# Kernel tuning notes

Measured on AMD Instinct MI355X. Metric: run time of the kernel, lower is better.

The kernel has to match this reference:

```python
import jax, jax.numpy as jnp
import numpy as np

EPS = 1e-5
NUM_GROUPS = 8


def group_norm(x, gamma, beta):
    # x: [B, C, T]; normalize per group over (C/G, T)
    B, C, T = x.shape
    G = NUM_GROUPS
    xg = x.reshape(B, G, C // G, T)
    mean = xg.mean(axis=(2, 3), keepdims=True)
    var = xg.var(axis=(2, 3), keepdims=True)
    xn = ((xg - mean) * jax.lax.rsqrt(var + EPS)).reshape(B, C, T)
    return xn * gamma[None, :, None] + beta[None, :, None]


def mish(x):
    return x * jnp.tanh(jax.nn.softplus(x))


def setup_inputs() -> dict:
    key = jax.random.key(0)
    ks = jax.random.split(key, 7)
    C, Cb, B, T = 1024, 256, 64, 512
    # conv1d kernel_size=1 weights stored as [out, in]
    w_down = jax.random.normal(ks[0], (Cb, C), dtype=jnp.float32) / np.sqrt(C)
    b_down = jax.random.normal(ks[1], (Cb,), dtype=jnp.float32) * 0.01
    w_up = jax.random.normal(ks[2], (C, Cb), dtype=jnp.float32) / np.sqrt(Cb)
    b_up = jax.random.normal(ks[3], (C,), dtype=jnp.float32) * 0.01
    gamma = jnp.ones((C,), dtype=jnp.float32)
    beta = jnp.zeros((C,), dtype=jnp.float32)
    x = jax.random.normal(ks[4], (B, C, T), dtype=jnp.float32)
    return {"x": x, "gamma": gamma, "beta": beta,
            "w_down": w_down, "b_down": b_down,
            "w_up": w_up, "b_up": b_up}


def reference(x, gamma, beta, w_down, b_down, w_up, b_up):
    residual = x
    h = group_norm(x, gamma, beta)                       # [B, C, T]
    h = jnp.einsum('bct,oc->bot', h, w_down) + b_down[None, :, None]  # [B, Cb, T]
    h = mish(h)
    h = jnp.einsum('bct,oc->bot', h, w_up) + b_up[None, :, None]      # [B, C, T]
    return h + residual
```

## Files before the change

### kernel.cpp

```cpp
#include <hip/hip_runtime.h>
#include <hip/hip_bf16.h>
#include <stddef.h>

#define B_   64
#define C_   1024
#define CB_  256
#define T_   512
#define G_   8
#define N_   32768
#define EPS_ 1e-5f

using short8  = __attribute__((ext_vector_type(8))) short;
using short4v = __attribute__((ext_vector_type(4))) short;
using f32x4   = __attribute__((ext_vector_type(4))) float;

__device__ __forceinline__ short f2bf(float f) {
    unsigned u = __float_as_uint(f);
    u += 0x7fffu + ((u >> 16) & 1u);
    return (short)(u >> 16);
}

__device__ __forceinline__ float mish_f(float y) {
    float u = __expf(fminf(y, 30.f));
    float w = u * u + 2.f * u;
    return y * (w / (w + 2.f));
}

__global__ void prep_weights(const float* __restrict__ wd, const float* __restrict__ wu,
                             short* __restrict__ wdb, short* __restrict__ wut) {
    int i = blockIdx.x * 256 + threadIdx.x;
    if (i < CB_ * C_) {
        wdb[i] = f2bf(wd[i]);
        int m = i >> 8, k = i & 255;
        int idx = (((m >> 4) * 8 + (k >> 5)) << 9) + (((k >> 3) & 3) << 7)
                + ((m & 15) << 3) + (k & 7);
        wut[idx] = f2bf(wu[i]);
    }
}

__global__ void stats_kernel(const float* __restrict__ x, const float* __restrict__ gamma,
                             const float* __restrict__ beta,
                             float* __restrict__ scaleW, float* __restrict__ shiftW) {
    const int tid = threadIdx.x;
    const int bg = blockIdx.x;
    const int b = bg >> 3, g = bg & 7;
    const float4* p = (const float4*)(x + ((size_t)b * C_ + g * 128) * T_);
    float s = 0.f, q = 0.f;
    for (int i = tid; i < 16384; i += 256) {
        float4 v = p[i];
        s += v.x + v.y + v.z + v.w;
        q += v.x * v.x + v.y * v.y + v.z * v.z + v.w * v.w;
    }
    for (int o = 32; o > 0; o >>= 1) {
        s += __shfl_down(s, o);
        q += __shfl_down(q, o);
    }
    __shared__ float red[8];
    __shared__ float mr[2];
    const int wid = tid >> 6, lane = tid & 63;
    if (lane == 0) { red[wid] = s; red[4 + wid] = q; }
    __syncthreads();
    if (tid == 0) {
        float S = red[0] + red[1] + red[2] + red[3];
        float Q = red[4] + red[5] + red[6] + red[7];
        float mean = S * (1.f / 65536.f);
        float var = Q * (1.f / 65536.f) - mean * mean;
        mr[0] = mean;
        mr[1] = rsqrtf(var + EPS_);
    }
    __syncthreads();
    float mean = mr[0], rstd = mr[1];
    if (tid < 128) {
        int c = g * 128 + tid;
        float sc = rstd * gamma[c];
        scaleW[b * C_ + c] = sc;
        shiftW[b * C_ + c] = beta[c] - mean * sc;
    }
}

#define LDSTR 40
#define MSTR  264

__global__ __launch_bounds__(512, 2) void fused_adapter(
    const float* __restrict__ x, const short* __restrict__ wd,
    const float* __restrict__ b_down,
    const float* __restrict__ scaleW, const float* __restrict__ shiftW,
    const short* __restrict__ wut, const float* __restrict__ b_up,
    float* __restrict__ out) {
    __shared__ short As[256 * LDSTR];
    __shared__ short Bs[128 * LDSTR];
    __shared__ float sS[C_], sT[C_];
    __shared__ short Ms[128 * MSTR];

    const int tid = threadIdx.x;
    const int n0 = blockIdx.x * 128;
    const int b  = n0 >> 9;
    const int t0 = n0 & 511;

    for (int i = tid; i < C_; i += 512) {
        sS[i] = scaleW[b * C_ + i];
        sT[i] = shiftW[b * C_ + i];
    }

    const int a_kc = tid & 3;
    const int a_m  = tid >> 2;
    const int b_n  = tid & 127;
    const int b_kg = tid >> 7;
    const int wid  = tid >> 6;
    const int lane = tid & 63;
    const int wm = wid >> 1, wn = wid & 1;
    const int q = lane >> 4, l16 = lane & 15;

    f32x4 acc[4][4];
#pragma unroll
    for (int i = 0; i < 4; i++)
#pragma unroll
        for (int j = 0; j < 4; j++) acc[i][j] = 0.f;

    const float* xb = x + (size_t)b * C_ * T_ + t0;

    short8 a0, a1;
    float bv[8];
    {
        const short* src = wd + a_m * C_ + a_kc * 8;
        a0 = *(const short8*)src;
        a1 = *(const short8*)(src + 128 * C_);
        const float* xp = xb + (size_t)(b_kg * 8) * T_ + b_n;
#pragma unroll
        for (int i = 0; i < 8; i++) bv[i] = xp[(size_t)i * T_];
    }
    __syncthreads();
    {
        *(short8*)&As[a_m * LDSTR + a_kc * 8] = a0;
        *(short8*)&As[(a_m + 128) * LDSTR + a_kc * 8] = a1;
        short8 v;
        const int kb = b_kg * 8;
#pragma unroll
        for (int i = 0; i < 8; i++) v[i] = f2bf(bv[i] * sS[kb + i] + sT[kb + i]);
        *(short8*)&Bs[b_n * LDSTR + kb] = v;
    }
    __syncthreads();

    for (int kt = 0; kt < 32; ++kt) {
        if (kt < 31) {
            const int k1 = (kt + 1) * 32;
            const short* src = wd + a_m * C_ + k1 + a_kc * 8;
            a0 = *(const short8*)src;
            a1 = *(const short8*)(src + 128 * C_);
            const float* xp = xb + (size_t)(k1 + b_kg * 8) * T_ + b_n;
#pragma unroll
            for (int i = 0; i < 8; i++) bv[i] = xp[(size_t)i * T_];
        }
        short8 af[4], bfr[4];
#pragma unroll
        for (int i = 0; i < 4; i++)
            af[i] = *(const short8*)&As[(wm * 64 + i * 16 + l16) * LDSTR + q * 8];
#pragma unroll
        for (int j = 0; j < 4; j++)
            bfr[j] = *(const short8*)&Bs[(wn * 64 + j * 16 + l16) * LDSTR + q * 8];
#pragma unroll
        for (int i = 0; i < 4; i++)
#pragma unroll
            for (int j = 0; j < 4; j++)
                acc[i][j] = __builtin_amdgcn_mfma_f32_16x16x32_bf16(af[i], bfr[j], acc[i][j], 0, 0, 0);
        __syncthreads();
        if (kt < 31) {
            *(short8*)&As[a_m * LDSTR + a_kc * 8] = a0;
            *(short8*)&As[(a_m + 128) * LDSTR + a_kc * 8] = a1;
            short8 v;
            const int kb = (kt + 1) * 32 + b_kg * 8;
            const int kl = b_kg * 8;
#pragma unroll
            for (int i = 0; i < 8; i++) v[i] = f2bf(bv[i] * sS[kb + i] + sT[kb + i]);
            *(short8*)&Bs[b_n * LDSTR + kl] = v;
        }
        __syncthreads();
    }

#pragma unroll
    for (int i = 0; i < 4; i++) {
        const int o_b = wm * 64 + i * 16 + q * 4;
        const float bd0 = b_down[o_b];
        const float bd1 = b_down[o_b + 1];
        const float bd2 = b_down[o_b + 2];
        const float bd3 = b_down[o_b + 3];
#pragma unroll
        for (int j = 0; j < 4; j++) {
            const int nl = wn * 64 + j * 16 + l16;
            short4v v;
            v[0] = f2bf(mish_f(acc[i][j][0] + bd0));
            v[1] = f2bf(mish_f(acc[i][j][1] + bd1));
            v[2] = f2bf(mish_f(acc[i][j][2] + bd2));
            v[3] = f2bf(mish_f(acc[i][j][3] + bd3));
            *(short4v*)&Ms[nl * MSTR + o_b] = v;
        }
    }
    __syncthreads();

#pragma unroll 1
    for (int half = 0; half < 2; ++half) {
        f32x4 a2[4][8];
#pragma unroll
        for (int i = 0; i < 4; i++)
#pragma unroll
            for (int j = 0; j < 8; j++) a2[i][j] = 0.f;

        const int mbb = half * 32 + wid * 4;
#pragma unroll 2
        for (int kt = 0; kt < 8; ++kt) {
            short8 af[4], bf2[8];
#pragma unroll
            for (int i = 0; i < 4; i++)
                af[i] = *(const short8*)(wut + ((size_t)((mbb + i) * 8 + kt) << 9) + lane * 8);
#pragma unroll
            for (int j = 0; j < 8; j++)
                bf2[j] = *(const short8*)&Ms[(j * 16 + l16) * MSTR + kt * 32 + q * 8];
#pragma unroll
            for (int i = 0; i < 4; i++)
#pragma unroll
                for (int j = 0; j < 8; j++)
                    a2[i][j] = __builtin_amdgcn_mfma_f32_16x16x32_bf16(af[i], bf2[j], a2[i][j], 0, 0, 0);
        }

#pragma unroll
        for (int i = 0; i < 4; i++) {
            const int c_b = half * 512 + wid * 64 + i * 16 + q * 4;
            const float bu0 = b_up[c_b];
            const float bu1 = b_up[c_b + 1];
            const float bu2 = b_up[c_b + 2];
            const float bu3 = b_up[c_b + 3];
#pragma unroll
            for (int j = 0; j < 8; j++) {
                const int tt = t0 + j * 16 + l16;
                const size_t gi = ((size_t)b * C_ + c_b) * T_ + tt;
                out[gi]              = a2[i][j][0] + bu0 + x[gi];
                out[gi + T_]         = a2[i][j][1] + bu1 + x[gi + T_];
                out[gi + 2 * T_]     = a2[i][j][2] + bu2 + x[gi + 2 * T_];
                out[gi + 3 * T_]     = a2[i][j][3] + bu3 + x[gi + 3 * T_];
            }
        }
    }
}

extern "C" void kernel_launch(void* const* d_in, const int* in_sizes, int n_in,
                              void* d_out, int out_size, void* d_ws, size_t ws_size,
                              hipStream_t stream) {
    const float* x      = (const float*)d_in[0];
    const float* gamma  = (const float*)d_in[1];
    const float* beta   = (const float*)d_in[2];
    const float* w_down = (const float*)d_in[3];
    const float* b_down = (const float*)d_in[4];
    const float* w_up   = (const float*)d_in[5];
    const float* b_up   = (const float*)d_in[6];
    float* out = (float*)d_out;

    float* scaleW = (float*)d_ws;
    float* shiftW = scaleW + B_ * C_;
    short* wdb    = (short*)(shiftW + B_ * C_);
    short* wut    = wdb + CB_ * C_;

    prep_weights<<<dim3((CB_ * C_ + 255) / 256), 256, 0, stream>>>(w_down, w_up, wdb, wut);
    stats_kernel<<<dim3(B_ * G_), 256, 0, stream>>>(x, gamma, beta, scaleW, shiftW);
    fused_adapter<<<dim3(N_ / 128), 512, 0, stream>>>(x, wdb, b_down, scaleW, shiftW,
                                                      wut, b_up, out);
}
```

Before: 317.4 us.

## Double-buffer LDS tiles in down-projection GEMM with two-stage global prefetch

Splits the A/B shared-memory tiles of the first GEMM into two buffers. Global loads are issued two k-steps ahead, and the next tile is written to the alternate buffer while MFMAs read the current one. This cuts the barriers per k-step from two to one. The barrier macro waits only on LDS counters, not global loads, so in-flight prefetches can stay outstanding across it. The cost is more LDS and a second set of prefetch registers, which may add register pressure under the 512-thread launch bound.

```diff
diff --git a/kernel.cpp b/kernel.cpp
--- a/kernel.cpp
+++ b/kernel.cpp
@@ -81,14 +81,18 @@
 #define LDSTR 40
 #define MSTR  264
 
+#define BAR() { asm volatile("s_waitcnt lgkmcnt(0)" ::: "memory"); __builtin_amdgcn_s_barrier(); }
+
 __global__ __launch_bounds__(512, 2) void fused_adapter(
     const float* __restrict__ x, const short* __restrict__ wd,
     const float* __restrict__ b_down,
     const float* __restrict__ scaleW, const float* __restrict__ shiftW,
     const short* __restrict__ wut, const float* __restrict__ b_up,
     float* __restrict__ out) {
-    __shared__ short As[256 * LDSTR];
-    __shared__ short Bs[128 * LDSTR];
+    __shared__ short As0[256 * LDSTR];
+    __shared__ short As1[256 * LDSTR];
+    __shared__ short Bs0[128 * LDSTR];
+    __shared__ short Bs1[128 * LDSTR];
     __shared__ float sS[C_], sT[C_];
     __shared__ short Ms[128 * MSTR];
 
@@ -119,62 +123,50 @@
 
     const float* xb = x + (size_t)b * C_ * T_ + t0;
 
-    short8 a0, a1;
-    float bv[8];
-    {
-        const short* src = wd + a_m * C_ + a_kc * 8;
-        a0 = *(const short8*)src;
-        a1 = *(const short8*)(src + 128 * C_);
-        const float* xp = xb + (size_t)(b_kg * 8) * T_ + b_n;
-#pragma unroll
-        for (int i = 0; i < 8; i++) bv[i] = xp[(size_t)i * T_];
-    }
-    __syncthreads();
-    {
-        *(short8*)&As[a_m * LDSTR + a_kc * 8] = a0;
-        *(short8*)&As[(a_m + 128) * LDSTR + a_kc * 8] = a1;
-        short8 v;
-        const int kb = b_kg * 8;
-#pragma unroll
-        for (int i = 0; i < 8; i++) v[i] = f2bf(bv[i] * sS[kb + i] + sT[kb + i]);
-        *(short8*)&Bs[b_n * LDSTR + kb] = v;
-    }
-    __syncthreads();
-
-    for (int kt = 0; kt < 32; ++kt) {
-        if (kt < 31) {
-            const int k1 = (kt + 1) * 32;
-            const short* src = wd + a_m * C_ + k1 + a_kc * 8;
-            a0 = *(const short8*)src;
-            a1 = *(const short8*)(src + 128 * C_);
-            const float* xp = xb + (size_t)(k1 + b_kg * 8) * T_ + b_n;
-#pragma unroll
-            for (int i = 0; i < 8; i++) bv[i] = xp[(size_t)i * T_];
-        }
-        short8 af[4], bfr[4];
-#pragma unroll
-        for (int i = 0; i < 4; i++)
-            af[i] = *(const short8*)&As[(wm * 64 + i * 16 + l16) * LDSTR + q * 8];
-#pragma unroll
-        for (int j = 0; j < 4; j++)
-            bfr[j] = *(const short8*)&Bs[(wn * 64 + j * 16 + l16) * LDSTR + q * 8];
-#pragma unroll
-        for (int i = 0; i < 4; i++)
-#pragma unroll
-            for (int j = 0; j < 4; j++)
-                acc[i][j] = __builtin_amdgcn_mfma_f32_16x16x32_bf16(af[i], bfr[j], acc[i][j], 0, 0, 0);
-        __syncthreads();
-        if (kt < 31) {
-            *(short8*)&As[a_m * LDSTR + a_kc * 8] = a0;
-            *(short8*)&As[(a_m + 128) * LDSTR + a_kc * 8] = a1;
-            short8 v;
-            const int kb = (kt + 1) * 32 + b_kg * 8;
-            const int kl = b_kg * 8;
-#pragma unroll
-            for (int i = 0; i < 8; i++) v[i] = f2bf(bv[i] * sS[kb + i] + sT[kb + i]);
-            *(short8*)&Bs[b_n * LDSTR + kl] = v;
-        }
-        __syncthreads();
+#define ISSUE(kt, aa0, aa1, bb) { \
+    const short* src = wd + a_m * C_ + (kt) * 32 + a_kc * 8; \
+    aa0 = *(const short8*)src; \
+    aa1 = *(const short8*)(src + 128 * C_); \
+    const float* xp = xb + (size_t)((kt) * 32 + b_kg * 8) * T_ + b_n; \
+    _Pragma("unroll") for (int i_ = 0; i_ < 8; i_++) bb[i_] = xp[(size_t)i_ * T_]; }
+
+#define STORE(kt, As_, Bs_, aa0, aa1, bb) { \
+    *(short8*)&As_[a_m * LDSTR + a_kc * 8] = aa0; \
+    *(short8*)&As_[(a_m + 128) * LDSTR + a_kc * 8] = aa1; \
+    const int kb_ = (kt) * 32 + b_kg * 8; \
+    short8 v_; \
+    _Pragma("unroll") for (int i_ = 0; i_ < 8; i_++) v_[i_] = f2bf(bb[i_] * sS[kb_ + i_] + sT[kb_ + i_]); \
+    *(short8*)&Bs_[b_n * LDSTR + b_kg * 8] = v_; }
+
+#define MFMA_STEP(As_, Bs_) { \
+    short8 af_[4], bf_[4]; \
+    _Pragma("unroll") for (int i_ = 0; i_ < 4; i_++) \
+        af_[i_] = *(const short8*)&As_[(wm * 64 + i_ * 16 + l16) * LDSTR + q * 8]; \
+    _Pragma("unroll") for (int j_ = 0; j_ < 4; j_++) \
+        bf_[j_] = *(const short8*)&Bs_[(wn * 64 + j_ * 16 + l16) * LDSTR + q * 8]; \
+    _Pragma("unroll") for (int i_ = 0; i_ < 4; i_++) \
+    _Pragma("unroll") for (int j_ = 0; j_ < 4; j_++) \
+        acc[i_][j_] = __builtin_amdgcn_mfma_f32_16x16x32_bf16(af_[i_], bf_[j_], acc[i_][j_], 0, 0, 0); }
+
+    short8 a0A, a1A, a0B, a1B;
+    float bvA[8], bvB[8];
+    ISSUE(0, a0A, a1A, bvA);
+    ISSUE(1, a0B, a1B, bvB);
+    BAR();
+    STORE(0, As0, Bs0, a0A, a1A, bvA);
+    BAR();
+
+#pragma unroll 1
+    for (int kt2 = 0; kt2 < 16; ++kt2) {
+        const int kt = kt2 * 2;
+        if (kt + 2 < 32) ISSUE(kt + 2, a0A, a1A, bvA);
+        MFMA_STEP(As0, Bs0);
+        STORE(kt + 1, As1, Bs1, a0B, a1B, bvB);
+        BAR();
+        if (kt + 3 < 32) ISSUE(kt + 3, a0B, a1B, bvB);
+        MFMA_STEP(As1, Bs1);
+        if (kt + 2 < 32) STORE(kt + 2, As0, Bs0, a0A, a1A, bvA);
+        BAR();
     }
 
 #pragma unroll
@@ -195,7 +187,7 @@
             *(short4v*)&Ms[nl * MSTR + o_b] = v;
         }
     }
-    __syncthreads();
+    BAR();
 
 #pragma unroll 1
     for (int half = 0; half < 2; ++half) {
@@ -240,6 +232,9 @@
             }
         }
     }
+#undef ISSUE
+#undef STORE
+#undef MFMA_STEP
 }
 
 extern "C" void kernel_launch(void* const* d_in, const int* in_sizes, int n_in,
```

After: 320.0 us. Within noise of the previous version (+0.8%).
